# Performance work log

Hardware: AMD Instinct MI355X
Metric: run time of the kernel (lower is better)

Reference implementation:

```python
import jax, jax.numpy as jnp
import numpy as np

B, N, M, D = 4, 16384, 4096, 64


def setup_inputs() -> dict:
    key = jax.random.key(0)
    k1, k2, k3 = jax.random.split(key, 3)
    pointcloud = jax.random.normal(k1, (B, N, 3), dtype=jnp.float32)
    keys = jax.random.normal(k2, (M, 3), dtype=jnp.float32)
    values = jax.random.normal(k3, (M, D), dtype=jnp.float32)
    return {"pointcloud": pointcloud, "keys": keys, "values": values}


def reference(pointcloud, keys, values):
    # Nearest-key quantization: argmin over squared L2 distances.
    # Expand ||p - k||^2 = ||p||^2 - 2 p.k + ||k||^2 (GEMM form; avoids the
    # (B,N,M,3) broadcasted diff tensor of the original).
    p_sq = jnp.sum(pointcloud * pointcloud, axis=-1, keepdims=True)      # (B,N,1)
    k_sq = jnp.sum(keys * keys, axis=-1)                                  # (M,)
    cross = jnp.einsum('bnc,mc->bnm', pointcloud, keys)                   # (B,N,M)
    d2 = p_sq - 2.0 * cross + k_sq[None, None, :]                         # (B,N,M)
    ids = jnp.argmin(d2, axis=-1)                                         # (B,N) int
    # Embedding lookup (get_features): gather rows of the value table.
    feats = values[ids]                                                   # (B,N,D)
    return feats, ids[..., None], pointcloud
```

## Files before the change

kernel.cpp:

```cpp
#include <hip/hip_runtime.h>

#pragma clang fp contract(off)

static __device__ __forceinline__ float min3f(float a, float b, float c) {
    float d;
    asm("v_min3_f32 %0, %1, %2, %3" : "=v"(d) : "v"(a), "v"(b), "v"(c));
    return d;
}

#define MM 4096
#define DD 64
#define BN 65536
#define FEATS_OFF 0
#define IDS_OFF (BN * DD)
#define PC_OFF (IDS_OFF + BN)

#define BLK 512
#define CC 32
#define PP 4
#define PPB 64
#define NPAIR (MM / 2)
#define KIT (MM / (2 * CC))

__global__ __launch_bounds__(BLK) __attribute__((amdgpu_waves_per_eu(4, 4)))
void quant_embed_kernel(const float* __restrict__ pc,
                        const float* __restrict__ keys,
                        const float* __restrict__ values,
                        float* __restrict__ out)
{
#pragma clang fp contract(off)
    __shared__ float4 skA[NPAIR];
    __shared__ float4 skB[NPAIR];

    const int tid = threadIdx.x;

    #pragma unroll
    for (int i = 0; i < NPAIR / BLK; ++i) {
        const int j = tid + i * BLK;
        const float2 f0 = ((const float2*)keys)[3 * j + 0];
        const float2 f1 = ((const float2*)keys)[3 * j + 1];
        const float2 f2 = ((const float2*)keys)[3 * j + 2];
        const float ksq0 = ((f0.x * f0.x) + (f0.y * f0.y)) + (f1.x * f1.x);
        const float ksq1 = ((f1.y * f1.y) + (f2.x * f2.x)) + (f2.y * f2.y);
        skA[j] = make_float4(-2.0f * f0.x, -2.0f * f1.y,
                             -2.0f * f0.y, -2.0f * f2.x);
        skB[j] = make_float4(-2.0f * f1.x, -2.0f * f2.y, ksq0, ksq1);
    }

    {
        const int base = blockIdx.x * (PPB * 3 / 4);
        if (tid < PPB * 3 / 4) {
            ((float4*)(out + PC_OFF))[base + tid] =
                ((const float4*)pc)[base + tid];
        }
    }

    const int c = tid & (CC - 1);
    const int g = tid >> 5;
    const int p0 = blockIdx.x * PPB + g * PP;

    float arr[12];
    {
        const float4* pcv = (const float4*)(pc + 3 * p0);
        #pragma unroll
        for (int i = 0; i < 3; ++i) ((float4*)arr)[i] = pcv[i];
    }
    float PX[PP], PY[PP], PZ[PP], PSQ[PP];
    float bd[PP];
    int bk[PP];
    #pragma unroll
    for (int i = 0; i < PP; ++i) {
        PX[i] = arr[3 * i + 0];
        PY[i] = arr[3 * i + 1];
        PZ[i] = arr[3 * i + 2];
        PSQ[i] = ((PX[i] * PX[i]) + (PY[i] * PY[i])) + (PZ[i] * PZ[i]);
        bd[i] = 3.402823466e38f;
        bk[i] = 0;
    }

    __syncthreads();

    #pragma unroll 2
    for (int k = 0; k < KIT; ++k) {
        const int j = (k << 5) + c;
        const float4 A  = skA[j];
        const float4 Bv = skB[j];
        #pragma unroll
        for (int i = 0; i < PP; ++i) {
            const float t0 = ((PX[i] * A.x) + (PY[i] * A.z)) + (PZ[i] * Bv.x);
            const float d0 = (PSQ[i] + t0) + Bv.z;
            const float t1 = ((PX[i] * A.y) + (PY[i] * A.w)) + (PZ[i] * Bv.y);
            const float d1 = (PSQ[i] + t1) + Bv.w;
            const float nb = min3f(bd[i], d0, d1);
            const bool ch = nb < bd[i];
            bd[i] = nb;
            bk[i] = ch ? k : bk[i];
        }
    }

    int bm[PP];
    #pragma unroll
    for (int i = 0; i < PP; ++i) {
        const int j = (bk[i] << 5) + c;
        const float4 A  = skA[j];
        const float4 Bv = skB[j];
        const float ca = ((PX[i] * A.x) + (PY[i] * A.z)) + (PZ[i] * Bv.x);
        const float da = (PSQ[i] + ca) + Bv.z;
        const int m0 = (bk[i] << 6) + (c << 1);
        float d = bd[i];
        int   m = (da == bd[i]) ? m0 : (m0 + 1);
        #pragma unroll
        for (int off = 1; off < CC; off <<= 1) {
            const float od = __shfl_xor(d, off);
            const int   om = __shfl_xor(m, off);
            if (od < d || (od == d && om < m)) { d = od; m = om; }
        }
        bm[i] = m;
    }

    #pragma unroll
    for (int i = 0; i < PP; ++i) {
        const float2* vrow = (const float2*)(values + (size_t)bm[i] * DD);
        ((float2*)(out + FEATS_OFF + (size_t)(p0 + i) * DD))[c] = vrow[c];
        if (c == 0) out[IDS_OFF + p0 + i] = (float)bm[i];
    }
}

extern "C" void kernel_launch(void* const* d_in, const int* in_sizes, int n_in,
                              void* d_out, int out_size, void* d_ws, size_t ws_size,
                              hipStream_t stream) {
    const float* pc     = (const float*)d_in[0];
    const float* keys   = (const float*)d_in[1];
    const float* values = (const float*)d_in[2];
    float* out = (float*)d_out;

    dim3 grid(BN / PPB);
    dim3 block(BLK);
    quant_embed_kernel<<<grid, block, 0, stream>>>(pc, keys, values, out);
}
```

Before: 113.8 us.

## Split keys across waves with scalar key loads and LDS cross-wave argmin

Reassigns the work so each lane owns 4 points and each of 16 waves scans a contiguous chunk of keys. Keys are read with wave-uniform (scalar-friendly) global loads instead of being staged in LDS. Partial minima are merged across waves through shared memory, and the feature copy then uses full 64-lane coalesced rows. This removes the per-block key staging and the LDS key reads from the hot loop. In exchange it adds an extra reduction pass with two barriers and uses 1024-thread blocks with fewer blocks overall.

```diff
diff --git a/kernel.cpp b/kernel.cpp
--- a/kernel.cpp
+++ b/kernel.cpp
@@ -15,114 +15,139 @@
 #define IDS_OFF (BN * DD)
 #define PC_OFF (IDS_OFF + BN)
 
-#define BLK 512
-#define CC 32
+#define BLK 1024
+#define WV 16
 #define PP 4
-#define PPB 64
-#define NPAIR (MM / 2)
-#define KIT (MM / (2 * CC))
+#define PTB (64 * PP)
+#define NBLK (BN / PTB)
+#define KCH (MM / WV)
+#define NG (KCH / 4)
 
-__global__ __launch_bounds__(BLK) __attribute__((amdgpu_waves_per_eu(4, 4)))
+__global__ __launch_bounds__(BLK)
 void quant_embed_kernel(const float* __restrict__ pc,
                         const float* __restrict__ keys,
                         const float* __restrict__ values,
                         float* __restrict__ out)
 {
 #pragma clang fp contract(off)
-    __shared__ float4 skA[NPAIR];
-    __shared__ float4 skB[NPAIR];
+    __shared__ float md[WV * PTB];
+    __shared__ int   mi[WV * PTB];
 
     const int tid = threadIdx.x;
-
-    #pragma unroll
-    for (int i = 0; i < NPAIR / BLK; ++i) {
-        const int j = tid + i * BLK;
-        const float2 f0 = ((const float2*)keys)[3 * j + 0];
-        const float2 f1 = ((const float2*)keys)[3 * j + 1];
-        const float2 f2 = ((const float2*)keys)[3 * j + 2];
-        const float ksq0 = ((f0.x * f0.x) + (f0.y * f0.y)) + (f1.x * f1.x);
-        const float ksq1 = ((f1.y * f1.y) + (f2.x * f2.x)) + (f2.y * f2.y);
-        skA[j] = make_float4(-2.0f * f0.x, -2.0f * f1.y,
-                             -2.0f * f0.y, -2.0f * f2.x);
-        skB[j] = make_float4(-2.0f * f1.x, -2.0f * f2.y, ksq0, ksq1);
-    }
+    const int l = tid & 63;
+    const int w = __builtin_amdgcn_readfirstlane(tid >> 6);
+    const int pbase = blockIdx.x * PTB;
 
     {
-        const int base = blockIdx.x * (PPB * 3 / 4);
-        if (tid < PPB * 3 / 4) {
+        const int base = blockIdx.x * (PTB * 3 / 4);
+        if (tid < PTB * 3 / 4) {
             ((float4*)(out + PC_OFF))[base + tid] =
                 ((const float4*)pc)[base + tid];
         }
     }
 
-    const int c = tid & (CC - 1);
-    const int g = tid >> 5;
-    const int p0 = blockIdx.x * PPB + g * PP;
-
-    float arr[12];
-    {
-        const float4* pcv = (const float4*)(pc + 3 * p0);
-        #pragma unroll
-        for (int i = 0; i < 3; ++i) ((float4*)arr)[i] = pcv[i];
-    }
-    float PX[PP], PY[PP], PZ[PP], PSQ[PP];
-    float bd[PP];
-    int bk[PP];
+    float PX[PP], PY[PP], PZ[PP], PSQ[PP], bd[PP];
+    int bg[PP];
     #pragma unroll
     for (int i = 0; i < PP; ++i) {
-        PX[i] = arr[3 * i + 0];
-        PY[i] = arr[3 * i + 1];
-        PZ[i] = arr[3 * i + 2];
-        PSQ[i] = ((PX[i] * PX[i]) + (PY[i] * PY[i])) + (PZ[i] * PZ[i]);
+        const int p = pbase + i * 64 + l;
+        const float px = pc[3 * p + 0];
+        const float py = pc[3 * p + 1];
+        const float pz = pc[3 * p + 2];
+        PX[i] = px; PY[i] = py; PZ[i] = pz;
+        PSQ[i] = ((px * px) + (py * py)) + (pz * pz);
         bd[i] = 3.402823466e38f;
-        bk[i] = 0;
+        bg[i] = 0;
     }
 
-    __syncthreads();
-
+    const float4* kv4 = (const float4*)keys;
+    const int gbase = w * NG;
     #pragma unroll 2
-    for (int k = 0; k < KIT; ++k) {
-        const int j = (k << 5) + c;
-        const float4 A  = skA[j];
-        const float4 Bv = skB[j];
+    for (int t = 0; t < NG; ++t) {
+        const int G = gbase + t;
+        const float4 ka = kv4[3 * G + 0];
+        const float4 kb = kv4[3 * G + 1];
+        const float4 kc = kv4[3 * G + 2];
+        const float kx0 = ka.x, ky0 = ka.y, kz0 = ka.z;
+        const float kx1 = ka.w, ky1 = kb.x, kz1 = kb.y;
+        const float kx2 = kb.z, ky2 = kb.w, kz2 = kc.x;
+        const float kx3 = kc.y, ky3 = kc.z, kz3 = kc.w;
+        const float tx0 = -2.0f * kx0, ty0 = -2.0f * ky0, tz0 = -2.0f * kz0;
+        const float tx1 = -2.0f * kx1, ty1 = -2.0f * ky1, tz1 = -2.0f * kz1;
+        const float tx2 = -2.0f * kx2, ty2 = -2.0f * ky2, tz2 = -2.0f * kz2;
+        const float tx3 = -2.0f * kx3, ty3 = -2.0f * ky3, tz3 = -2.0f * kz3;
+        const float ts0 = ((kx0 * kx0) + (ky0 * ky0)) + (kz0 * kz0);
+        const float ts1 = ((kx1 * kx1) + (ky1 * ky1)) + (kz1 * kz1);
+        const float ts2 = ((kx2 * kx2) + (ky2 * ky2)) + (kz2 * kz2);
+        const float ts3 = ((kx3 * kx3) + (ky3 * ky3)) + (kz3 * kz3);
         #pragma unroll
         for (int i = 0; i < PP; ++i) {
-            const float t0 = ((PX[i] * A.x) + (PY[i] * A.z)) + (PZ[i] * Bv.x);
-            const float d0 = (PSQ[i] + t0) + Bv.z;
-            const float t1 = ((PX[i] * A.y) + (PY[i] * A.w)) + (PZ[i] * Bv.y);
-            const float d1 = (PSQ[i] + t1) + Bv.w;
-            const float nb = min3f(bd[i], d0, d1);
+            const float c0 = ((PX[i] * tx0) + (PY[i] * ty0)) + (PZ[i] * tz0);
+            const float d0 = (PSQ[i] + c0) + ts0;
+            const float c1 = ((PX[i] * tx1) + (PY[i] * ty1)) + (PZ[i] * tz1);
+            const float d1 = (PSQ[i] + c1) + ts1;
+            const float c2 = ((PX[i] * tx2) + (PY[i] * ty2)) + (PZ[i] * tz2);
+            const float d2 = (PSQ[i] + c2) + ts2;
+            const float c3 = ((PX[i] * tx3) + (PY[i] * ty3)) + (PZ[i] * tz3);
+            const float d3 = (PSQ[i] + c3) + ts3;
+            float nb = min3f(bd[i], d0, d1);
+            nb = min3f(nb, d2, d3);
             const bool ch = nb < bd[i];
             bd[i] = nb;
-            bk[i] = ch ? k : bk[i];
+            bg[i] = ch ? t : bg[i];
         }
     }
 
     int bm[PP];
     #pragma unroll
     for (int i = 0; i < PP; ++i) {
-        const int j = (bk[i] << 5) + c;
-        const float4 A  = skA[j];
-        const float4 Bv = skB[j];
-        const float ca = ((PX[i] * A.x) + (PY[i] * A.z)) + (PZ[i] * Bv.x);
-        const float da = (PSQ[i] + ca) + Bv.z;
-        const int m0 = (bk[i] << 6) + (c << 1);
-        float d = bd[i];
-        int   m = (da == bd[i]) ? m0 : (m0 + 1);
+        const int G = gbase + bg[i];
+        const float4 ka = kv4[3 * G + 0];
+        const float4 kb = kv4[3 * G + 1];
+        const float4 kc = kv4[3 * G + 2];
+        const float kxq[4] = {ka.x, ka.w, kb.z, kc.y};
+        const float kyq[4] = {ka.y, kb.x, kb.w, kc.z};
+        const float kzq[4] = {ka.z, kb.y, kc.x, kc.w};
+        int m = 4 * G + 3;
         #pragma unroll
-        for (int off = 1; off < CC; off <<= 1) {
-            const float od = __shfl_xor(d, off);
-            const int   om = __shfl_xor(m, off);
-            if (od < d || (od == d && om < m)) { d = od; m = om; }
+        for (int q = 3; q >= 0; --q) {
+            const float tx = -2.0f * kxq[q];
+            const float ty = -2.0f * kyq[q];
+            const float tz = -2.0f * kzq[q];
+            const float ts = ((kxq[q] * kxq[q]) + (kyq[q] * kyq[q])) + (kzq[q] * kzq[q]);
+            const float cr = ((PX[i] * tx) + (PY[i] * ty)) + (PZ[i] * tz);
+            const float dq = (PSQ[i] + cr) + ts;
+            if (dq == bd[i]) m = 4 * G + q;
         }
         bm[i] = m;
     }
 
     #pragma unroll
     for (int i = 0; i < PP; ++i) {
-        const float2* vrow = (const float2*)(values + (size_t)bm[i] * DD);
-        ((float2*)(out + FEATS_OFF + (size_t)(p0 + i) * DD))[c] = vrow[c];
-        if (c == 0) out[IDS_OFF + p0 + i] = (float)bm[i];
+        md[w * PTB + i * 64 + l] = bd[i];
+        mi[w * PTB + i * 64 + l] = bm[i];
+    }
+    __syncthreads();
+    if (tid < PTB) {
+        float d = md[tid];
+        int   m = mi[tid];
+        #pragma unroll
+        for (int ww = 1; ww < WV; ++ww) {
+            const float od = md[ww * PTB + tid];
+            const int   om = mi[ww * PTB + tid];
+            if (od < d || (od == d && om < m)) { d = od; m = om; }
+        }
+        mi[tid] = m;
+        out[IDS_OFF + pbase + tid] = (float)m;
+    }
+    __syncthreads();
+
+    #pragma unroll
+    for (int r = 0; r < PTB / WV; ++r) {
+        const int p = w * (PTB / WV) + r;
+        const int mm = mi[p];
+        out[FEATS_OFF + (size_t)(pbase + p) * DD + l] =
+            values[(size_t)mm * DD + l];
     }
 }
 
@@ -134,7 +159,7 @@
     const float* values = (const float*)d_in[2];
     float* out = (float*)d_out;
 
-    dim3 grid(BN / PPB);
+    dim3 grid(NBLK);
     dim3 block(BLK);
     quant_embed_kernel<<<grid, block, 0, stream>>>(pc, keys, values, out);
 }
```

Measured after the change: 144.5 us. 26.9% more time.
